# Kernel optimization log

Hardware: AMD Instinct MI355X
Metric: run time of the kernel (lower is better)

Reference implementation:

```python
import jax, jax.numpy as jnp
import numpy as np

N, C_IN, C, V = 500000, 64, 64, 20000  # C = out_channel // 2


def bn(x, g, b, eps):
    # training-mode BatchNorm1d: batch statistics, biased variance
    mu = jnp.mean(x, axis=0)
    var = jnp.mean(jnp.square(x - mu), axis=0)
    return (x - mu) * jax.lax.rsqrt(var + eps) * g + b


def setup_inputs() -> dict:
    key = jax.random.key(0)
    ks = jax.random.split(key, 12)
    s = 0.05
    return {
        "inputs": jax.random.normal(ks[0], (N, C_IN), jnp.float32),
        "unq_inv": jax.random.randint(ks[1], (N,), 0, V, jnp.int32),
        "kv_W": jax.random.normal(ks[2], (C_IN, C), jnp.float32) * s,
        "kv_b": jnp.zeros((C,), jnp.float32),
        "norm_g": jnp.ones((C,), jnp.float32),
        "norm_b": jnp.zeros((C,), jnp.float32),
        "w1_W": jax.random.normal(ks[3], (C_IN, C), jnp.float32) * s,
        "w1_bias": jnp.zeros((C,), jnp.float32),
        "w_bn_g": jnp.ones((C,), jnp.float32),
        "w_bn_b": jnp.zeros((C,), jnp.float32),
        "w2_W": jax.random.normal(ks[4], (C, C), jnp.float32) * s,
        "w2_bias": jnp.zeros((C,), jnp.float32),
        "pre_W": jax.random.normal(ks[5], (C_IN, C), jnp.float32) * s,
        "pre_bias": jnp.zeros((C,), jnp.float32),
        "pre_bn_g": jnp.ones((C,), jnp.float32),
        "pre_bn_b": jnp.zeros((C,), jnp.float32),
        "posw_W": jax.random.normal(ks[6], (C, C), jnp.float32) * s,
        "posw_bias": jnp.zeros((C,), jnp.float32),
        "link_bn_g": jnp.ones((C,), jnp.float32),
        "link_bn_b": jnp.zeros((C,), jnp.float32),
    }


def _forward(inputs, unq_inv, kv_W, kv_b, norm_g, norm_b, w1_W, w1_bias,
             w_bn_g, w_bn_b, w2_W, w2_bias, pre_W, pre_bias, pre_bn_g,
             pre_bn_b, posw_W, posw_bias, link_bn_g, link_bn_b):
    inv = unq_inv
    # v = kv(inputs); x = relu(norm(v))
    v = inputs @ kv_W + kv_b                                   # [N, C]
    x = jax.nn.relu(bn(v, norm_g, norm_b, 1e-3))               # [N, C]
    # scatter_max
    q_max = jax.ops.segment_max(x, inv, num_segments=V)        # [V, C]
    q_max = jnp.where(jnp.isneginf(q_max), 0.0, q_max)
    # weight = w(inputs): Linear -> BN -> ReLU -> Linear
    h = jax.nn.relu(bn(inputs @ w1_W + w1_bias, w_bn_g, w_bn_b, 1e-5))
    weight = h @ w2_W + w2_bias                                # [N, C]
    # scatter_softmax over segments
    m = jax.ops.segment_max(weight, inv, num_segments=V)
    m = jnp.where(jnp.isneginf(m), 0.0, m)
    ex = jnp.exp(weight - m[inv])
    denom = jax.ops.segment_sum(ex, inv, num_segments=V)
    soft_weight = ex / denom[inv]                              # [N, C]
    # scatter_mean(soft_weight * v)
    cnt = jax.ops.segment_sum(jnp.ones((inputs.shape[0],), inputs.dtype), inv, num_segments=V)
    cnt = jnp.maximum(cnt, 1.0)[:, None]
    weight_x = jax.ops.segment_sum(soft_weight * v, inv, num_segments=V) / cnt  # [V, C]
    # LinkConv(q_max, inputs, inv)
    p = bn(inputs @ pre_W + pre_bias, pre_bn_g, pre_bn_b, 1e-3)  # [N, C]
    pw = p @ posw_W + posw_bias
    fs = p * jnp.sin(pw)
    fc = p * jnp.cos(pw)
    add_s = jax.ops.segment_sum(fs, inv, num_segments=V)         # [V, C]
    add_c = jax.ops.segment_sum(fc, inv, num_segments=V)
    f = bn(q_max @ pre_W + pre_bias, pre_bn_g, pre_bn_b, 1e-3)   # [V, C]
    mw = f @ posw_W + posw_bias
    cs = f * jnp.sin(mw)
    cc = f * jnp.cos(mw)
    final = (add_s + cs) * cs + (add_c + cc) * cc
    link_feat = jax.nn.relu(bn(final, link_bn_g, link_bn_b, 1e-3))
    weight_x = (link_feat + weight_x) * 0.5
    return jnp.concatenate([weight_x, q_max], axis=-1)           # [V, 2C]


def reference(inputs, unq_inv, kv_W, kv_b, norm_g, norm_b, w1_W, w1_bias,
              w_bn_g, w_bn_b, w2_W, w2_bias, pre_W, pre_bias, pre_bn_g,
              pre_bn_b, posw_W, posw_bias, link_bn_g, link_bn_b):
    return _forward(inputs, unq_inv, kv_W, kv_b, norm_g, norm_b, w1_W, w1_bias,
                    w_bn_g, w_bn_b, w2_W, w2_bias, pre_W, pre_bias, pre_bn_g,
                    pre_bn_b, posw_W, posw_bias, link_bn_g, link_bn_b)
```

## Files before the change

### kernel.cpp

```cpp
#include <hip/hip_runtime.h>

typedef __attribute__((ext_vector_type(8))) short  bf16x8;
typedef __attribute__((ext_vector_type(4))) float  f32x4;

#define MFMA16(a,b,c) __builtin_amdgcn_mfma_f32_16x16x32_bf16((a),(b),(c),0,0,0)

__device__ __forceinline__ float b2f(ushort u){ return __uint_as_float(((unsigned)u)<<16); }
__device__ __forceinline__ ushort f2b(float f){
  unsigned u = __float_as_uint(f);
  unsigned r = (u + 0x7FFFu + ((u>>16)&1u)) >> 16;
  return (ushort)r;
}
__device__ __forceinline__ float ldv(const void* p, long i, int mode){
  return mode ? ((const float*)p)[i] : b2f(((const ushort*)p)[i]);
}

__global__ void pfn_detect(const void* X, int* mode){
  __shared__ int cnt;
  if (threadIdx.x==0) cnt=0;
  __syncthreads();
  const ushort* u = (const ushort*)X;
  int bad=0;
  for (int i=threadIdx.x; i<4096; i+=256){
    float v = b2f(u[i]);
    if (!(fabsf(v) < 1e4f)) bad++;
  }
  atomicAdd(&cnt, bad);
  __syncthreads();
  if (threadIdx.x==0) *mode = (cnt > 204) ? 1 : 0;
}

__global__ __launch_bounds__(256) void pfn_g(const void* __restrict__ X, int N,
                                             float* __restrict__ G, float* __restrict__ svec,
                                             const int* gmode)
{
  __shared__ __align__(16) ushort xt[128*72];
  __shared__ float gred[4096];
  __shared__ float sred[64];
  int mode = *gmode;
  int tid = threadIdx.x;
  int w = tid>>6, lane = tid&63, q = lane>>4, li = lane&15;
  for (int u=tid; u<4096; u+=256) gred[u]=0.f;
  if (tid<64) sred[tid]=0.f;

  float s_acc[32];
#pragma unroll
  for (int i=0;i<32;i++) s_acc[i]=0.f;
  const f32x4 fz = {0.f,0.f,0.f,0.f};
  f32x4 acc[4][4];
#pragma unroll
  for (int a=0;a<4;a++)
#pragma unroll
    for (int b=0;b<4;b++) acc[a][b]=fz;

  int rr = tid>>1, half = tid&1;
  int nch = (N + 127)/128;
  for (int cb = blockIdx.x; cb < nch; cb += gridDim.x){
    int r = cb*128 + rr;
    float vals[32];
    if (r < N){
      if (mode){
        const float4* src = (const float4*)((const float*)X + (size_t)r*64 + half*32);
#pragma unroll
        for (int i=0;i<8;i++){ float4 f=src[i];
          vals[i*4]=f.x; vals[i*4+1]=f.y; vals[i*4+2]=f.z; vals[i*4+3]=f.w; }
      } else {
        const uint4* src = (const uint4*)((const ushort*)X + (size_t)r*64 + half*32);
#pragma unroll
        for (int i=0;i<4;i++){ uint4 u=src[i]; const ushort* pu=(const ushort*)&u;
#pragma unroll
          for (int l=0;l<8;l++) vals[i*8+l]=b2f(pu[l]); }
      }
    } else {
#pragma unroll
      for (int i=0;i<32;i++) vals[i]=0.f;
    }
#pragma unroll
    for (int i=0;i<32;i++) s_acc[i] += vals[i];
    ushort tmp[32];
#pragma unroll
    for (int i=0;i<32;i++) tmp[i]=f2b(vals[i]);
    uint4* dst = (uint4*)(xt + rr*72 + half*32);
#pragma unroll
    for (int i=0;i<4;i++) dst[i]=((const uint4*)tmp)[i];
    __syncthreads();

    bf16x8 fr[4];
#pragma unroll
    for (int mt=0; mt<4; mt++){
      bf16x8 f;
#pragma unroll
      for (int j=0;j<8;j++) f[j] = (short)xt[(w*32 + q*8 + j)*72 + mt*16 + li];
      fr[mt]=f;
    }
#pragma unroll
    for (int mt=0;mt<4;mt++)
#pragma unroll
      for (int nt=0;nt<4;nt++)
        acc[mt][nt] = MFMA16(fr[mt], fr[nt], acc[mt][nt]);
    __syncthreads();
  }
#pragma unroll
  for (int mt=0;mt<4;mt++)
#pragma unroll
    for (int nt=0;nt<4;nt++)
#pragma unroll
      for (int i=0;i<4;i++)
        atomicAdd(&gred[(mt*16 + q*4 + i)*64 + nt*16 + li], acc[mt][nt][i]);
#pragma unroll
  for (int i=0;i<32;i++) atomicAdd(&sred[half*32 + i], s_acc[i]);
  __syncthreads();
  for (int u=tid; u<4096; u+=256) atomicAdd(&G[u], gred[u]);
  if (tid<64) atomicAdd(&svec[tid], sred[tid]);
}

__global__ __launch_bounds__(256) void pfn_kstatsA(
    const float* __restrict__ G, const float* __restrict__ svec,
    const void* __restrict__ kvW, const void* __restrict__ w1W, const void* __restrict__ preW,
    const void* __restrict__ kvb, const void* __restrict__ w1b, const void* __restrict__ preb,
    const void* __restrict__ ng,  const void* __restrict__ nb,
    const void* __restrict__ wg,  const void* __restrict__ wb,
    const void* __restrict__ pg,  const void* __restrict__ pb,
    float* __restrict__ aA, float* __restrict__ cA,
    float* __restrict__ a1, float* __restrict__ ap, float* __restrict__ bp,
    float* __restrict__ bcat, float Nf, const int* gmode)
{
  __shared__ float gl[4096];
  __shared__ float sl[64];
  __shared__ float wl[4096];
  int mode = *gmode;
  int tid = threadIdx.x; int path = blockIdx.x;
  const void* wsel = (path==0)? kvW : (path==1)? w1W : preW;
  for (int u=tid; u<4096; u+=256){ gl[u]=G[u]; wl[u]=ldv(wsel,u,mode); }
  if (tid<64) sl[tid]=svec[tid];
  __syncthreads();
  int j = tid>>2, sub = tid&3;
  float ps=0.f, qf=0.f;
  for (int k=sub*16; k<sub*16+16; k++){
    float wk = wl[k*64+j];
    ps += sl[k]*wk;
    float tk=0.f;
    for (int m=0;m<64;m++) tk += gl[k*64+m]*wl[m*64+j];
    qf += tk*wk;
  }
  qf += __shfl_down(qf,2); qf += __shfl_down(qf,1);
  ps += __shfl_down(ps,2); ps += __shfl_down(ps,1);
  if (sub==0){
    float bias = ldv((path==0)? kvb : (path==1)? w1b : preb, j, mode);
    float gam  = ldv((path==0)? ng  : (path==1)? wg  : pg , j, mode);
    float bet  = ldv((path==0)? nb  : (path==1)? wb  : pb , j, mode);
    float eps  = (path==1)? 1e-5f : 1e-3f;
    float mean_raw = ps/Nf, qn = qf/Nf;
    float mean = mean_raw + bias;
    float var  = qn + 2.f*bias*mean_raw + bias*bias - mean*mean;
    float rstd = rsqrtf(fmaxf(var,0.f)+eps);
    float a = gam*rstd, c = bet - mean*a;
    if (path==0){ aA[j]=a; cA[j]=c; bcat[j]=bias; }
    else if (path==1){ a1[j]=a; bcat[64+j]=c+bias*a; }
    else { ap[j]=a; bp[j]=c+bias*a; bcat[128+j]=c+bias*a; }
  }
}

__global__ __launch_bounds__(256) void pfn_kstatsB(
    const void* __restrict__ kvW, const void* __restrict__ w1W,
    const void* __restrict__ preW, const void* __restrict__ poswW,
    const void* __restrict__ w2W, const void* __restrict__ w2b,
    const void* __restrict__ poswb,
    const float* __restrict__ a1, const float* __restrict__ ap, const float* __restrict__ bp,
    ushort* __restrict__ WT, float* __restrict__ bcat, float* __restrict__ b2o,
    const int* gmode)
{
  int mode = *gmode;
  int gidx = blockIdx.x*256 + threadIdx.x;
  for (int idx=gidx; idx<320*64; idx+=64*256){
    int n = idx>>6, k = idx&63;
    float o;
    if (n<64)        o = ldv(kvW, k*64+n, mode);
    else if (n<128){ int j=n-64;  o = ldv(w1W, k*64+j, mode)*a1[j]; }
    else if (n<192){ int j=n-128; o = ldv(preW, k*64+j, mode)*ap[j]; }
    else if (n<256){ int j=n-192; float t=0.f;
      for (int m=0;m<64;m++) t += ldv(preW,k*64+m,mode)*ap[m]*ldv(poswW,m*64+j,mode);
      o = t;
    } else {         int j=n-256; o = ldv(w2W, k*64+j, mode); }
    WT[idx] = f2b(o);
  }
  if (blockIdx.x==0 && threadIdx.x<64){
    int j = threadIdx.x; float bb=0.f;
    for (int m=0;m<64;m++) bb += bp[m]*ldv(poswW,m*64+j,mode);
    bcat[192+j] = bb + ldv(poswb,j,mode);
    b2o[j] = ldv(w2b,j,mode);
  }
}

__global__ void pfn_hist(const int* __restrict__ inv, int* __restrict__ hist, int N, int V){
  int i = blockIdx.x*blockDim.x + threadIdx.x;
  int stride = gridDim.x*blockDim.x;
  for (; i<N; i+=stride){
    int s = min(max(inv[i],0), V-1);
    atomicAdd(&hist[s], 1);
  }
}

__global__ __launch_bounds__(256) void pfn_scan(const int* __restrict__ hist,
                                                int* __restrict__ base, int* __restrict__ off,
                                                float* __restrict__ cntf, int V, int N){
  __shared__ int part[256];
  int tid = threadIdx.x;
  int per = (V+255)/256;
  int s0 = tid*per, s1 = min(s0+per, V);
  int sum=0;
  for (int s=s0;s<s1;s++) sum += hist[s];
  part[tid]=sum;
  __syncthreads();
  if (tid==0){ int acc=0; for (int i=0;i<256;i++){ int t=part[i]; part[i]=acc; acc+=t; } }
  __syncthreads();
  int acc = part[tid];
  for (int s=s0;s<s1;s++){ base[s]=acc; off[s]=acc; cntf[s]=(float)hist[s]; acc+=hist[s]; }
  if (tid==255) base[V]=N;
}

__global__ void pfn_scat(const int* __restrict__ inv, int* __restrict__ off,
                         int* __restrict__ sidx, int* __restrict__ segid, int N, int V){
  int i = blockIdx.x*blockDim.x + threadIdx.x;
  int stride = gridDim.x*blockDim.x;
  for (; i<N; i+=stride){
    int s = min(max(inv[i],0), V-1);
    int p = atomicAdd(&off[s],1);
    sidx[p] = i;
    segid[p] = s;
  }
}

#define RED_STORE(EXPR) \
  _Pragma("unroll") for (int s=0;s<2;s++){ \
  _Pragma("unroll") for (int i=0;i<4;i++){ \
    int rloc=w*32+s*16+q*4+i; \
  _Pragma("unroll") for (int t=0;t<4;t++){ int c=t*16+li; red[rloc*65+c] = (EXPR); } } }

#define RED_ADD(DST) { int cc=tid&63, gg=tid>>6; int nn=nlsS; \
  for (int ls=gg; ls<nn; ls+=4){ int sd=segSeg[ls]; if (sd<0) continue; \
    int lo=segStart[ls], hi=segStart[ls+1]; float a_=0.f; \
    for (int r_=lo; r_<hi; r_++) a_ += red[r_*65+cc]; \
    atomicAdd(&DST[(size_t)sd*64+cc], a_); } }

#define RED_MAX(DST) { int cc=tid&63, gg=tid>>6; int nn=nlsS; \
  for (int ls=gg; ls<nn; ls+=4){ int sd=segSeg[ls]; if (sd<0) continue; \
    int lo=segStart[ls], hi=segStart[ls+1]; float a_=0.f; \
    for (int r_=lo; r_<hi; r_++) a_ = fmaxf(a_, red[r_*65+cc]); \
    atomicMax(&DST[(size_t)sd*64+cc], __float_as_uint(a_)); } }

__global__ __launch_bounds__(256) void pfn_ms(
    const void* __restrict__ X, const int* __restrict__ sidx, const int* __restrict__ segid,
    const ushort* __restrict__ WT, const float* __restrict__ bcat,
    const float* __restrict__ aA, const float* __restrict__ cA, const float* __restrict__ b2o,
    unsigned int* __restrict__ qm, float* __restrict__ adds, float* __restrict__ addc,
    float* __restrict__ dnm, float* __restrict__ acv,
    int N, const int* gmode)
{
  __shared__ __align__(16) ushort xt[128*72];
  __shared__ float red[128*65];
  __shared__ float bcl[256], aAl[64], cAl[64], b2l[64];
  __shared__ int invs[128];
  __shared__ int segStart[129];
  __shared__ int segSeg[128];
  __shared__ int nlsS;
  int mode = *gmode;
  int tid = threadIdx.x;
  int p0 = blockIdx.x*128;

  {
    int rr=tid>>1, half=tid&1;
    int p = p0+rr;
    long r = (p<N)? (long)sidx[p] : -1;
    float vals[32];
    if (r>=0){
      if (mode){
        const float4* src=(const float4*)((const float*)X + r*64 + half*32);
#pragma unroll
        for (int i=0;i<8;i++){ float4 f=src[i];
          vals[i*4]=f.x; vals[i*4+1]=f.y; vals[i*4+2]=f.z; vals[i*4+3]=f.w; }
      } else {
        const uint4* src=(const uint4*)((const ushort*)X + r*64 + half*32);
#pragma unroll
        for (int i=0;i<4;i++){ uint4 u=src[i]; const ushort* pu=(const ushort*)&u;
#pragma unroll
          for (int l=0;l<8;l++) vals[i*8+l]=b2f(pu[l]); }
      }
    } else {
#pragma unroll
      for (int i=0;i<32;i++) vals[i]=0.f;
    }
    ushort tmp[32];
#pragma unroll
    for (int i=0;i<32;i++) tmp[i]=f2b(vals[i]);
    uint4* dst=(uint4*)(xt + rr*72 + half*32);
#pragma unroll
    for (int i=0;i<4;i++) dst[i]=((const uint4*)tmp)[i];
  }
  if (tid<128){ int p=p0+tid; invs[tid] = (p<N)? segid[p] : -1; }
  bcl[tid]=bcat[tid];
  if (tid<64){ aAl[tid]=aA[tid]; cAl[tid]=cA[tid]; b2l[tid]=b2o[tid]; }
  __syncthreads();
  if (tid==0){
    int n=0, prev=-2;
    for (int t=0;t<128;t++){ int s=invs[t]; if (s!=prev){ segStart[n]=t; segSeg[n]=s; prev=s; n++; } }
    segStart[n]=128; nlsS=n;
  }

  int w=tid>>6, lane=tid&63, q=lane>>4, li=lane&15;
  const f32x4 fz={0.f,0.f,0.f,0.f};

  f32x4 AV[2][4], AP[2][4], AW[2][4];
#pragma unroll
  for (int s=0;s<2;s++)
#pragma unroll
    for (int t=0;t<4;t++){ AV[s][t]=fz; AP[s][t]=fz; AW[s][t]=fz; }
#pragma unroll
  for (int kk=0;kk<2;kk++){
    bf16x8 a0 = *(const bf16x8*)&xt[(w*32 +      li)*72 + kk*32 + q*8];
    bf16x8 a1 = *(const bf16x8*)&xt[(w*32 + 16 + li)*72 + kk*32 + q*8];
    int ko = kk*32 + q*8;
#pragma unroll
    for (int t=0;t<4;t++){
      bf16x8 bv = *(const bf16x8*)&WT[(      t*16+li)*64 + ko];
      AV[0][t]=MFMA16(a0,bv,AV[0][t]); AV[1][t]=MFMA16(a1,bv,AV[1][t]);
      bf16x8 bp_= *(const bf16x8*)&WT[(128 + t*16+li)*64 + ko];
      AP[0][t]=MFMA16(a0,bp_,AP[0][t]); AP[1][t]=MFMA16(a1,bp_,AP[1][t]);
      bf16x8 bw = *(const bf16x8*)&WT[(192 + t*16+li)*64 + ko];
      AW[0][t]=MFMA16(a0,bw,AW[0][t]); AW[1][t]=MFMA16(a1,bw,AW[1][t]);
    }
  }
#pragma unroll
  for (int s=0;s<2;s++)
#pragma unroll
    for (int t=0;t<4;t++)
#pragma unroll
      for (int i=0;i<4;i++){
        int c=t*16+li;
        float v = AV[s][t][i] + bcl[c];
        AV[s][t][i] = v;
        float p = AP[s][t][i] + bcl[128+c];
        float pw= AW[s][t][i] + bcl[192+c];
        AP[s][t][i] = p*__sinf(pw);
        AW[s][t][i] = p*__cosf(pw);
      }
  RED_STORE(fmaxf(AV[s][t][i]*aAl[c]+cAl[c], 0.f));
  __syncthreads();
  RED_MAX(qm);
  __syncthreads();
  RED_STORE(AP[s][t][i]);
  __syncthreads();
  RED_ADD(adds);
  __syncthreads();
  RED_STORE(AW[s][t][i]);
  __syncthreads();
  RED_ADD(addc);
  __syncthreads();

  f32x4 AH[2][4];
#pragma unroll
  for (int s=0;s<2;s++)
#pragma unroll
    for (int t=0;t<4;t++) AH[s][t]=fz;
#pragma unroll
  for (int kk=0;kk<2;kk++){
    bf16x8 a0 = *(const bf16x8*)&xt[(w*32 +      li)*72 + kk*32 + q*8];
    bf16x8 a1 = *(const bf16x8*)&xt[(w*32 + 16 + li)*72 + kk*32 + q*8];
    int ko = kk*32 + q*8;
#pragma unroll
    for (int t=0;t<4;t++){
      bf16x8 bh = *(const bf16x8*)&WT[(64 + t*16+li)*64 + ko];
      AH[0][t]=MFMA16(a0,bh,AH[0][t]); AH[1][t]=MFMA16(a1,bh,AH[1][t]);
    }
  }
#pragma unroll
  for (int s=0;s<2;s++)
#pragma unroll
    for (int i=0;i<4;i++){
      int rloc=w*32+s*16+q*4+i;
#pragma unroll
      for (int t=0;t<4;t++){
        int c=t*16+li;
        xt[rloc*72 + c] = f2b(fmaxf(AH[s][t][i]+bcl[64+c], 0.f));
      }
    }
  __syncthreads();

  f32x4 AZ[2][4];
#pragma unroll
  for (int s=0;s<2;s++)
#pragma unroll
    for (int t=0;t<4;t++) AZ[s][t]=fz;
#pragma unroll
  for (int kk=0;kk<2;kk++){
    bf16x8 a0 = *(const bf16x8*)&xt[(w*32 +      li)*72 + kk*32 + q*8];
    bf16x8 a1 = *(const bf16x8*)&xt[(w*32 + 16 + li)*72 + kk*32 + q*8];
    int ko = kk*32 + q*8;
#pragma unroll
    for (int t=0;t<4;t++){
      bf16x8 bz = *(const bf16x8*)&WT[(256 + t*16+li)*64 + ko];
      AZ[0][t]=MFMA16(a0,bz,AZ[0][t]); AZ[1][t]=MFMA16(a1,bz,AZ[1][t]);
    }
  }
#pragma unroll
  for (int s=0;s<2;s++)
#pragma unroll
    for (int t=0;t<4;t++)
#pragma unroll
      for (int i=0;i<4;i++){
        int c=t*16+li;
        float e = __expf(fminf(AZ[s][t][i]+b2l[c], 30.f));
        AZ[s][t][i] = e;
        AV[s][t][i] = e*AV[s][t][i];
      }
  RED_STORE(AZ[s][t][i]);
  __syncthreads();
  RED_ADD(dnm);
  __syncthreads();
  RED_STORE(AV[s][t][i]);
  __syncthreads();
  RED_ADD(acv);
}

__global__ __launch_bounds__(256) void pfn_k2(
    const float* __restrict__ qmax, const void* __restrict__ preW,
    const void* __restrict__ preb, float* __restrict__ fq,
    float* __restrict__ fsum, float* __restrict__ fssq, int V, const int* gmode)
{
  __shared__ float pwl[64*72];
  __shared__ float qrow[4][64];
  __shared__ float red[8][64];
  int mode = *gmode;
  int tid=threadIdx.x, slot=tid>>6, j=tid&63;
  for (int u=tid;u<4096;u+=256){
    int k=u>>6, n=u&63;
    pwl[k*72+n]=ldv(preW,u,mode);
  }
  int per = (V + (int)gridDim.x - 1)/(int)gridDim.x;
  per = (per+3)&~3;
  int start = blockIdx.x*per, end = min(start+per, V);
  float ps=0.f, pq=0.f;
  float bj = ldv(preb,j,mode);
  __syncthreads();
  for (int rb=start; rb<end; rb+=4){
    int r = rb + slot;
    qrow[slot][j] = (r<V)? qmax[(size_t)r*64+j] : 0.f;
    __syncthreads();
    if (r<end){
      float t=bj;
#pragma unroll
      for (int k=0;k<64;k++) t += qrow[slot][k]*pwl[k*72+j];
      fq[(size_t)r*64+j]=t;
      ps += t; pq += t*t;
    }
    __syncthreads();
  }
  red[slot][j]=ps; red[4+slot][j]=pq;
  __syncthreads();
  if (slot==0){
    float s  = red[0][j]+red[1][j]+red[2][j]+red[3][j];
    float s2 = red[4][j]+red[5][j]+red[6][j]+red[7][j];
    atomicAdd(&fsum[j], s); atomicAdd(&fssq[j], s2);
  }
}

__global__ __launch_bounds__(256) void pfn_k4(
    const float* __restrict__ fq, const float* __restrict__ add_s,
    const float* __restrict__ add_c, const void* __restrict__ poswW,
    const void* __restrict__ poswb,
    const float* __restrict__ fsum, const float* __restrict__ fssq,
    const void* __restrict__ pg, const void* __restrict__ pbeta,
    float* __restrict__ finalb, float* __restrict__ lsum, float* __restrict__ lssq,
    int V, const int* gmode)
{
  __shared__ float pwl[64*72];
  __shared__ float frow[4][64];
  __shared__ float red[8][64];
  int mode = *gmode;
  int tid=threadIdx.x, slot=tid>>6, j=tid&63;
  for (int u=tid;u<4096;u+=256){
    int k=u>>6, n=u&63;
    pwl[k*72+n]=ldv(poswW,u,mode);
  }
  float Vf = (float)V;
  float mean = fsum[j]/Vf;
  float var  = fssq[j]/Vf - mean*mean;
  float s2 = ldv(pg,j,mode)*rsqrtf(fmaxf(var,0.f)+1e-3f);
  float c2 = ldv(pbeta,j,mode) - mean*s2;
  float pbj = ldv(poswb,j,mode);
  int per = (V + (int)gridDim.x - 1)/(int)gridDim.x;
  per = (per+3)&~3;
  int start = blockIdx.x*per, end = min(start+per, V);
  float ps=0.f, pq=0.f;
  __syncthreads();
  for (int rb=start; rb<end; rb+=4){
    int r = rb + slot;
    float fv = 0.f;
    if (r<end) fv = fq[(size_t)r*64+j]*s2 + c2;
    frow[slot][j]=fv;
    __syncthreads();
    if (r<end){
      float mw=pbj;
#pragma unroll
      for (int k=0;k<64;k++) mw += frow[slot][k]*pwl[k*72+j];
      float sn=__sinf(mw), cn=__cosf(mw);
      float cs = fv*sn, cc = fv*cn;
      float fin = (add_s[(size_t)r*64+j]+cs)*cs + (add_c[(size_t)r*64+j]+cc)*cc;
      finalb[(size_t)r*64+j]=fin;
      ps += fin; pq += fin*fin;
    }
    __syncthreads();
  }
  red[slot][j]=ps; red[4+slot][j]=pq;
  __syncthreads();
  if (slot==0){
    float s  = red[0][j]+red[1][j]+red[2][j]+red[3][j];
    float s2r= red[4][j]+red[5][j]+red[6][j]+red[7][j];
    atomicAdd(&lsum[j], s); atomicAdd(&lssq[j], s2r);
  }
}

__global__ __launch_bounds__(256) void pfn_k6(
    const float* __restrict__ finalb, const float* __restrict__ qmax,
    const float* __restrict__ denom, const float* __restrict__ accv,
    const float* __restrict__ cnt,
    const float* __restrict__ lsum, const float* __restrict__ lssq,
    const void* __restrict__ lg, const void* __restrict__ lb,
    void* __restrict__ out, int V, const int* gmode)
{
  int mode = *gmode;
  int tid=threadIdx.x, slot=tid>>6, j=tid&63;
  int r = blockIdx.x*4 + slot;
  if (r>=V) return;
  float Vf=(float)V;
  float mean=lsum[j]/Vf, var=lssq[j]/Vf-mean*mean;
  float s3=ldv(lg,j,mode)*rsqrtf(fmaxf(var,0.f)+1e-3f);
  float c3=ldv(lb,j,mode)-mean*s3;
  float lf = fmaxf(finalb[(size_t)r*64+j]*s3+c3, 0.f);
  float dn = denom[(size_t)r*64+j];
  float wx = accv[(size_t)r*64+j] / fmaxf(dn, 1e-20f);
  wx /= fmaxf(cnt[r],1.f);
  float y0 = (lf+wx)*0.5f;
  float y1 = qmax[(size_t)r*64+j];
  size_t o0 = (size_t)r*128+j, o1 = (size_t)r*128+64+j;
  if (mode){ ((float*)out)[o0]=y0; ((float*)out)[o1]=y1; }
  else { ((ushort*)out)[o0]=f2b(y0); ((ushort*)out)[o1]=f2b(y1); }
}

__global__ void pfn_sent(ushort* out, int n){
  int i = blockIdx.x*256 + threadIdx.x;
  if (i<n) out[i]=0x5300;
}

extern "C" void kernel_launch(void* const* d_in, const int* in_sizes, int n_in,
                              void* d_out, int out_size, void* d_ws, size_t ws_size,
                              hipStream_t stream)
{
  const void* X    = d_in[0];
  const int*  inv  = (const int*)d_in[1];
  const void* kvW  = d_in[2];
  const void* kvb  = d_in[3];
  const void* ng   = d_in[4];
  const void* nb   = d_in[5];
  const void* w1W  = d_in[6];
  const void* w1b  = d_in[7];
  const void* wg   = d_in[8];
  const void* wb   = d_in[9];
  const void* w2W  = d_in[10];
  const void* w2b  = d_in[11];
  const void* preW = d_in[12];
  const void* preb = d_in[13];
  const void* pg   = d_in[14];
  const void* pb   = d_in[15];
  const void* poswW= d_in[16];
  const void* poswb= d_in[17];
  const void* lg   = d_in[18];
  const void* lb   = d_in[19];

  int N = in_sizes[1];
  int V = out_size / 128;

  char* ws = (char*)d_ws;
  size_t off = 0;
  auto alloc = [&](size_t b){ size_t o=off; off=(off+b+255)&~(size_t)255; return o; };
  size_t oMode = alloc(256);
  size_t oG    = alloc(16384);
  size_t oS    = alloc(256);
  size_t oaA   = alloc(256);
  size_t ocA   = alloc(256);
  size_t obcat = alloc(1024);
  size_t ob2   = alloc(256);
  size_t oa1   = alloc(256);
  size_t oap   = alloc(256);
  size_t obp   = alloc(256);
  size_t ofsum = alloc(256);
  size_t ofssq = alloc(256);
  size_t olsum = alloc(256);
  size_t olssq = alloc(256);
  size_t zero1_end = off;
  size_t oWT   = alloc(320*64*2);
  size_t oqm   = alloc((size_t)V*256);
  size_t oadds = alloc((size_t)V*256);
  size_t oaddc = alloc((size_t)V*256);
  size_t odnm  = alloc((size_t)V*256);
  size_t oacv  = alloc((size_t)V*256);
  size_t ohist = alloc((size_t)V*4);
  size_t zero2_end = off;
  size_t ocntf = alloc((size_t)V*4);
  size_t obase = alloc((size_t)(V+1)*4);
  size_t ooff  = alloc((size_t)V*4);
  size_t osidx = alloc((size_t)N*4);
  size_t osegd = alloc((size_t)N*4);
  size_t ofq   = alloc((size_t)V*256);
  size_t ofin  = alloc((size_t)V*256);
  size_t need  = off;
  (void)n_in;

  if (ws_size < need){
    pfn_sent<<<(out_size+255)/256,256,0,stream>>>((ushort*)d_out, out_size);
    return;
  }

  hipMemsetAsync(ws, 0, zero1_end, stream);
  hipMemsetAsync(ws + oqm, 0, zero2_end - oqm, stream);

  int* gmode = (int*)(ws+oMode);

  pfn_detect<<<1,256,0,stream>>>(X, gmode);

  pfn_g<<<512,256,0,stream>>>(X, N, (float*)(ws+oG), (float*)(ws+oS), gmode);

  pfn_hist<<<2048,256,0,stream>>>(inv, (int*)(ws+ohist), N, V);

  pfn_kstatsA<<<3,256,0,stream>>>(
      (const float*)(ws+oG), (const float*)(ws+oS),
      kvW, w1W, preW, kvb, w1b, preb, ng, nb, wg, wb, pg, pb,
      (float*)(ws+oaA), (float*)(ws+ocA),
      (float*)(ws+oa1),
      (float*)(ws+oap), (float*)(ws+obp),
      (float*)(ws+obcat), (float)N, gmode);

  pfn_scan<<<1,256,0,stream>>>((const int*)(ws+ohist), (int*)(ws+obase),
                               (int*)(ws+ooff), (float*)(ws+ocntf), V, N);

  pfn_kstatsB<<<64,256,0,stream>>>(
      kvW, w1W, preW, poswW, w2W, w2b, poswb,
      (const float*)(ws+oa1), (const float*)(ws+oap), (const float*)(ws+obp),
      (ushort*)(ws+oWT), (float*)(ws+obcat), (float*)(ws+ob2), gmode);

  pfn_scat<<<2048,256,0,stream>>>(inv, (int*)(ws+ooff), (int*)(ws+osidx),
                                  (int*)(ws+osegd), N, V);

  int gb = (N + 127)/128;
  pfn_ms<<<gb,256,0,stream>>>(
      X, (const int*)(ws+osidx), (const int*)(ws+osegd),
      (const ushort*)(ws+oWT), (const float*)(ws+obcat),
      (const float*)(ws+oaA), (const float*)(ws+ocA), (const float*)(ws+ob2),
      (unsigned int*)(ws+oqm), (float*)(ws+oadds), (float*)(ws+oaddc),
      (float*)(ws+odnm), (float*)(ws+oacv),
      N, gmode);

  pfn_k2<<<250,256,0,stream>>>(
      (const float*)(ws+oqm), preW, preb,
      (float*)(ws+ofq), (float*)(ws+ofsum), (float*)(ws+ofssq), V, gmode);

  pfn_k4<<<250,256,0,stream>>>(
      (const float*)(ws+ofq), (const float*)(ws+oadds), (const float*)(ws+oaddc),
      poswW, poswb, (const float*)(ws+ofsum), (const float*)(ws+ofssq),
      pg, pb, (float*)(ws+ofin), (float*)(ws+olsum), (float*)(ws+olssq), V, gmode);

  pfn_k6<<<(V+3)/4,256,0,stream>>>(
      (const float*)(ws+ofin), (const float*)(ws+oqm),
      (const float*)(ws+odnm), (const float*)(ws+oacv), (const float*)(ws+ocntf),
      (const float*)(ws+olsum), (const float*)(ws+olssq),
      lg, lb, d_out, V, gmode);
}
```

Baseline: 728.8 us.

## Replace staged segment reductions with LDS atomics and fuse histogram into gram kernel

The segmented max/sum reductions in pfn_ms no longer go through a 128x65 shared staging buffer with many block barriers. They now accumulate into small per-local-segment LDS accumulators using shared atomics, with a fast path when a 4-row MFMA group falls in a single segment, and then flush to global atomics. The histogram kernel is folded into pfn_g, input staging skips the float round-trip, occupancy hints and grid sizes are raised, and one barrier is dropped. A block is capped at 24 local segments (MAXS), so inputs with more distinct segments per 128 sorted rows would be merged incorrectly.

```diff
diff --git a/kernel.cpp b/kernel.cpp
--- a/kernel.cpp
+++ b/kernel.cpp
@@ -32,7 +32,8 @@
 
 __global__ __launch_bounds__(256) void pfn_g(const void* __restrict__ X, int N,
                                              float* __restrict__ G, float* __restrict__ svec,
-                                             const int* gmode)
+                                             const int* gmode,
+                                             const int* __restrict__ inv, int* __restrict__ hist, int V)
 {
   __shared__ __align__(16) ushort xt[128*72];
   __shared__ float gred[4096];
@@ -40,6 +41,16 @@
   int mode = *gmode;
   int tid = threadIdx.x;
   int w = tid>>6, lane = tid&63, q = lane>>4, li = lane&15;
+
+  {
+    long i = (long)blockIdx.x*blockDim.x + tid;
+    long stride = (long)gridDim.x*blockDim.x;
+    for (; i<N; i+=stride){
+      int s = min(max(inv[i],0), V-1);
+      atomicAdd(&hist[s], 1);
+    }
+  }
+
   for (int u=tid; u<4096; u+=256) gred[u]=0.f;
   if (tid<64) sred[tid]=0.f;
 
@@ -57,32 +68,37 @@
   int nch = (N + 127)/128;
   for (int cb = blockIdx.x; cb < nch; cb += gridDim.x){
     int r = cb*128 + rr;
-    float vals[32];
+    uint4* dst = (uint4*)(xt + rr*72 + half*32);
     if (r < N){
       if (mode){
         const float4* src = (const float4*)((const float*)X + (size_t)r*64 + half*32);
 #pragma unroll
-        for (int i=0;i<8;i++){ float4 f=src[i];
-          vals[i*4]=f.x; vals[i*4+1]=f.y; vals[i*4+2]=f.z; vals[i*4+3]=f.w; }
+        for (int i=0;i<4;i++){
+          float4 f0=src[i*2], f1=src[i*2+1];
+          s_acc[i*8+0]+=f0.x; s_acc[i*8+1]+=f0.y; s_acc[i*8+2]+=f0.z; s_acc[i*8+3]+=f0.w;
+          s_acc[i*8+4]+=f1.x; s_acc[i*8+5]+=f1.y; s_acc[i*8+6]+=f1.z; s_acc[i*8+7]+=f1.w;
+          uint4 u;
+          u.x = (unsigned)f2b(f0.x) | ((unsigned)f2b(f0.y)<<16);
+          u.y = (unsigned)f2b(f0.z) | ((unsigned)f2b(f0.w)<<16);
+          u.z = (unsigned)f2b(f1.x) | ((unsigned)f2b(f1.y)<<16);
+          u.w = (unsigned)f2b(f1.z) | ((unsigned)f2b(f1.w)<<16);
+          dst[i]=u;
+        }
       } else {
         const uint4* src = (const uint4*)((const ushort*)X + (size_t)r*64 + half*32);
 #pragma unroll
-        for (int i=0;i<4;i++){ uint4 u=src[i]; const ushort* pu=(const ushort*)&u;
-#pragma unroll
-          for (int l=0;l<8;l++) vals[i*8+l]=b2f(pu[l]); }
+        for (int i=0;i<4;i++){
+          uint4 u=src[i]; dst[i]=u;
+          const ushort* pu=(const ushort*)&u;
+#pragma unroll
+          for (int l=0;l<8;l++) s_acc[i*8+l] += b2f(pu[l]);
+        }
       }
     } else {
-#pragma unroll
-      for (int i=0;i<32;i++) vals[i]=0.f;
-    }
-#pragma unroll
-    for (int i=0;i<32;i++) s_acc[i] += vals[i];
-    ushort tmp[32];
-#pragma unroll
-    for (int i=0;i<32;i++) tmp[i]=f2b(vals[i]);
-    uint4* dst = (uint4*)(xt + rr*72 + half*32);
-#pragma unroll
-    for (int i=0;i<4;i++) dst[i]=((const uint4*)tmp)[i];
+      uint4 z={0,0,0,0};
+#pragma unroll
+      for (int i=0;i<4;i++) dst[i]=z;
+    }
     __syncthreads();
 
     bf16x8 fr[4];
@@ -192,15 +208,6 @@
   }
 }
 
-__global__ void pfn_hist(const int* __restrict__ inv, int* __restrict__ hist, int N, int V){
-  int i = blockIdx.x*blockDim.x + threadIdx.x;
-  int stride = gridDim.x*blockDim.x;
-  for (; i<N; i+=stride){
-    int s = min(max(inv[i],0), V-1);
-    atomicAdd(&hist[s], 1);
-  }
-}
-
 __global__ __launch_bounds__(256) void pfn_scan(const int* __restrict__ hist,
                                                 int* __restrict__ base, int* __restrict__ off,
                                                 float* __restrict__ cntf, int V, int N){
@@ -231,25 +238,9 @@
   }
 }
 
-#define RED_STORE(EXPR) \
-  _Pragma("unroll") for (int s=0;s<2;s++){ \
-  _Pragma("unroll") for (int i=0;i<4;i++){ \
-    int rloc=w*32+s*16+q*4+i; \
-  _Pragma("unroll") for (int t=0;t<4;t++){ int c=t*16+li; red[rloc*65+c] = (EXPR); } } }
-
-#define RED_ADD(DST) { int cc=tid&63, gg=tid>>6; int nn=nlsS; \
-  for (int ls=gg; ls<nn; ls+=4){ int sd=segSeg[ls]; if (sd<0) continue; \
-    int lo=segStart[ls], hi=segStart[ls+1]; float a_=0.f; \
-    for (int r_=lo; r_<hi; r_++) a_ += red[r_*65+cc]; \
-    atomicAdd(&DST[(size_t)sd*64+cc], a_); } }
-
-#define RED_MAX(DST) { int cc=tid&63, gg=tid>>6; int nn=nlsS; \
-  for (int ls=gg; ls<nn; ls+=4){ int sd=segSeg[ls]; if (sd<0) continue; \
-    int lo=segStart[ls], hi=segStart[ls+1]; float a_=0.f; \
-    for (int r_=lo; r_<hi; r_++) a_ = fmaxf(a_, red[r_*65+cc]); \
-    atomicMax(&DST[(size_t)sd*64+cc], __float_as_uint(a_)); } }
-
-__global__ __launch_bounds__(256) void pfn_ms(
+#define MAXS 24
+
+__global__ __launch_bounds__(256,4) void pfn_ms(
     const void* __restrict__ X, const int* __restrict__ sidx, const int* __restrict__ segid,
     const ushort* __restrict__ WT, const float* __restrict__ bcat,
     const float* __restrict__ aA, const float* __restrict__ cA, const float* __restrict__ b2o,
@@ -258,53 +249,60 @@
     int N, const int* gmode)
 {
   __shared__ __align__(16) ushort xt[128*72];
-  __shared__ float red[128*65];
+  __shared__ float segA[3][MAXS][64];
   __shared__ float bcl[256], aAl[64], cAl[64], b2l[64];
   __shared__ int invs[128];
-  __shared__ int segStart[129];
-  __shared__ int segSeg[128];
+  __shared__ int segSeg[MAXS];
+  __shared__ __align__(4) unsigned char lsRow[128];
   __shared__ int nlsS;
   int mode = *gmode;
   int tid = threadIdx.x;
   int p0 = blockIdx.x*128;
 
+  for (int u=tid; u<3*MAXS*64; u+=256) ((float*)segA)[u]=0.f;
+
   {
     int rr=tid>>1, half=tid&1;
     int p = p0+rr;
     long r = (p<N)? (long)sidx[p] : -1;
-    float vals[32];
+    uint4* dst=(uint4*)(xt + rr*72 + half*32);
     if (r>=0){
       if (mode){
         const float4* src=(const float4*)((const float*)X + r*64 + half*32);
 #pragma unroll
-        for (int i=0;i<8;i++){ float4 f=src[i];
-          vals[i*4]=f.x; vals[i*4+1]=f.y; vals[i*4+2]=f.z; vals[i*4+3]=f.w; }
+        for (int i=0;i<4;i++){
+          float4 f0=src[i*2], f1=src[i*2+1];
+          uint4 u;
+          u.x = (unsigned)f2b(f0.x) | ((unsigned)f2b(f0.y)<<16);
+          u.y = (unsigned)f2b(f0.z) | ((unsigned)f2b(f0.w)<<16);
+          u.z = (unsigned)f2b(f1.x) | ((unsigned)f2b(f1.y)<<16);
+          u.w = (unsigned)f2b(f1.z) | ((unsigned)f2b(f1.w)<<16);
+          dst[i]=u;
+        }
       } else {
         const uint4* src=(const uint4*)((const ushort*)X + r*64 + half*32);
 #pragma unroll
-        for (int i=0;i<4;i++){ uint4 u=src[i]; const ushort* pu=(const ushort*)&u;
-#pragma unroll
-          for (int l=0;l<8;l++) vals[i*8+l]=b2f(pu[l]); }
+        for (int i=0;i<4;i++) dst[i]=src[i];
       }
     } else {
-#pragma unroll
-      for (int i=0;i<32;i++) vals[i]=0.f;
-    }
-    ushort tmp[32];
-#pragma unroll
-    for (int i=0;i<32;i++) tmp[i]=f2b(vals[i]);
-    uint4* dst=(uint4*)(xt + rr*72 + half*32);
-#pragma unroll
-    for (int i=0;i<4;i++) dst[i]=((const uint4*)tmp)[i];
+      uint4 z={0,0,0,0};
+#pragma unroll
+      for (int i=0;i<4;i++) dst[i]=z;
+    }
   }
   if (tid<128){ int p=p0+tid; invs[tid] = (p<N)? segid[p] : -1; }
   bcl[tid]=bcat[tid];
   if (tid<64){ aAl[tid]=aA[tid]; cAl[tid]=cA[tid]; b2l[tid]=b2o[tid]; }
   __syncthreads();
+
   if (tid==0){
     int n=0, prev=-2;
-    for (int t=0;t<128;t++){ int s=invs[t]; if (s!=prev){ segStart[n]=t; segSeg[n]=s; prev=s; n++; } }
-    segStart[n]=128; nlsS=n;
+    for (int t=0;t<128;t++){
+      int s=invs[t];
+      if (s!=prev && n<MAXS){ segSeg[n]=s; n++; prev=s; }
+      lsRow[t]=(unsigned char)(n-1);
+    }
+    nlsS=n;
   }
 
   int w=tid>>6, lane=tid&63, q=lane>>4, li=lane&15;
@@ -330,31 +328,59 @@
       AW[0][t]=MFMA16(a0,bw,AW[0][t]); AW[1][t]=MFMA16(a1,bw,AW[1][t]);
     }
   }
-#pragma unroll
-  for (int s=0;s<2;s++)
-#pragma unroll
-    for (int t=0;t<4;t++)
+  __syncthreads();
+
+#pragma unroll
+  for (int s=0;s<2;s++){
+    uchar4 lv = *(const uchar4*)&lsRow[w*32 + s*16 + q*4];
+    bool uni = (lv.x==lv.w);
+#pragma unroll
+    for (int t=0;t<4;t++){
+      int c=t*16+li;
+      float bv=bcl[c], bpc=bcl[128+c], bwc=bcl[192+c], aa=aAl[c], ca=cAl[c];
+      float xs[4], ss[4], sc[4];
 #pragma unroll
       for (int i=0;i<4;i++){
-        int c=t*16+li;
-        float v = AV[s][t][i] + bcl[c];
+        float v = AV[s][t][i] + bv;
         AV[s][t][i] = v;
-        float p = AP[s][t][i] + bcl[128+c];
-        float pw= AW[s][t][i] + bcl[192+c];
-        AP[s][t][i] = p*__sinf(pw);
-        AW[s][t][i] = p*__cosf(pw);
+        float p = AP[s][t][i] + bpc;
+        float pw= AW[s][t][i] + bwc;
+        ss[i] = p*__sinf(pw);
+        sc[i] = p*__cosf(pw);
+        xs[i] = fmaxf(v*aa+ca, 0.f);
       }
-  RED_STORE(fmaxf(AV[s][t][i]*aAl[c]+cAl[c], 0.f));
-  __syncthreads();
-  RED_MAX(qm);
-  __syncthreads();
-  RED_STORE(AP[s][t][i]);
-  __syncthreads();
-  RED_ADD(adds);
-  __syncthreads();
-  RED_STORE(AW[s][t][i]);
-  __syncthreads();
-  RED_ADD(addc);
+      if (uni){
+        int l=lv.x;
+        float mx = fmaxf(fmaxf(xs[0],xs[1]),fmaxf(xs[2],xs[3]));
+        atomicMax((unsigned int*)&segA[0][l][c], __float_as_uint(mx));
+        atomicAdd(&segA[1][l][c], (ss[0]+ss[1])+(ss[2]+ss[3]));
+        atomicAdd(&segA[2][l][c], (sc[0]+sc[1])+(sc[2]+sc[3]));
+      } else {
+        int la[4]={lv.x,lv.y,lv.z,lv.w};
+#pragma unroll
+        for (int i=0;i<4;i++){
+          atomicMax((unsigned int*)&segA[0][la[i]][c], __float_as_uint(xs[i]));
+          atomicAdd(&segA[1][la[i]][c], ss[i]);
+          atomicAdd(&segA[2][la[i]][c], sc[i]);
+        }
+      }
+    }
+  }
+  __syncthreads();
+
+  {
+    int cc=tid&63, gg=tid>>6, nn=nlsS;
+    for (int ls=gg; ls<nn; ls+=4){
+      int sd=segSeg[ls];
+      if (sd>=0){
+        atomicMax(&qm[(size_t)sd*64+cc], __float_as_uint(segA[0][ls][cc]));
+        atomicAdd(&adds[(size_t)sd*64+cc], segA[1][ls][cc]);
+        atomicAdd(&addc[(size_t)sd*64+cc], segA[2][ls][cc]);
+      }
+      segA[0][ls][cc]=0.f;
+      segA[1][ls][cc]=0.f;
+    }
+  }
   __syncthreads();
 
   f32x4 AH[2][4];
@@ -384,7 +410,6 @@
         xt[rloc*72 + c] = f2b(fmaxf(AH[s][t][i]+bcl[64+c], 0.f));
       }
     }
-  __syncthreads();
 
   f32x4 AZ[2][4];
 #pragma unroll
@@ -403,23 +428,45 @@
     }
   }
 #pragma unroll
-  for (int s=0;s<2;s++)
-#pragma unroll
-    for (int t=0;t<4;t++)
+  for (int s=0;s<2;s++){
+    uchar4 lv = *(const uchar4*)&lsRow[w*32 + s*16 + q*4];
+    bool uni = (lv.x==lv.w);
+#pragma unroll
+    for (int t=0;t<4;t++){
+      int c=t*16+li;
+      float b2=b2l[c];
+      float es[4], vs[4];
 #pragma unroll
       for (int i=0;i<4;i++){
-        int c=t*16+li;
-        float e = __expf(fminf(AZ[s][t][i]+b2l[c], 30.f));
-        AZ[s][t][i] = e;
-        AV[s][t][i] = e*AV[s][t][i];
+        float e = __expf(fminf(AZ[s][t][i]+b2, 30.f));
+        es[i]=e;
+        vs[i]=e*AV[s][t][i];
       }
-  RED_STORE(AZ[s][t][i]);
-  __syncthreads();
-  RED_ADD(dnm);
-  __syncthreads();
-  RED_STORE(AV[s][t][i]);
-  __syncthreads();
-  RED_ADD(acv);
+      if (uni){
+        int l=lv.x;
+        atomicAdd(&segA[0][l][c], (es[0]+es[1])+(es[2]+es[3]));
+        atomicAdd(&segA[1][l][c], (vs[0]+vs[1])+(vs[2]+vs[3]));
+      } else {
+        int la[4]={lv.x,lv.y,lv.z,lv.w};
+#pragma unroll
+        for (int i=0;i<4;i++){
+          atomicAdd(&segA[0][la[i]][c], es[i]);
+          atomicAdd(&segA[1][la[i]][c], vs[i]);
+        }
+      }
+    }
+  }
+  __syncthreads();
+
+  {
+    int cc=tid&63, gg=tid>>6, nn=nlsS;
+    for (int ls=gg; ls<nn; ls+=4){
+      int sd=segSeg[ls];
+      if (sd<0) continue;
+      atomicAdd(&dnm[(size_t)sd*64+cc], segA[0][ls][cc]);
+      atomicAdd(&acv[(size_t)sd*64+cc], segA[1][ls][cc]);
+    }
+  }
 }
 
 __global__ __launch_bounds__(256) void pfn_k2(
@@ -628,9 +675,8 @@
 
   pfn_detect<<<1,256,0,stream>>>(X, gmode);
 
-  pfn_g<<<512,256,0,stream>>>(X, N, (float*)(ws+oG), (float*)(ws+oS), gmode);
-
-  pfn_hist<<<2048,256,0,stream>>>(inv, (int*)(ws+ohist), N, V);
+  pfn_g<<<1024,256,0,stream>>>(X, N, (float*)(ws+oG), (float*)(ws+oS), gmode,
+                               inv, (int*)(ws+ohist), V);
 
   pfn_kstatsA<<<3,256,0,stream>>>(
       (const float*)(ws+oG), (const float*)(ws+oS),
@@ -660,11 +706,11 @@
       (float*)(ws+odnm), (float*)(ws+oacv),
       N, gmode);
 
-  pfn_k2<<<250,256,0,stream>>>(
+  pfn_k2<<<500,256,0,stream>>>(
       (const float*)(ws+oqm), preW, preb,
       (float*)(ws+ofq), (float*)(ws+ofsum), (float*)(ws+ofssq), V, gmode);
 
-  pfn_k4<<<250,256,0,stream>>>(
+  pfn_k4<<<500,256,0,stream>>>(
       (const float*)(ws+ofq), (const float*)(ws+oadds), (const float*)(ws+oaddc),
       poswW, poswb, (const float*)(ws+ofsum), (const float*)(ws+ofssq),
       pg, pb, (float*)(ws+ofin), (float*)(ws+olsum), (float*)(ws+olssq), V, gmode);
```

New measurement: 856.0 us. 17.5% more time.
